# Kernel optimization log

Measured on AMD Instinct MI355X. Metric: run time of the kernel, lower is better.

Reference implementation:

```python
import jax, jax.numpy as jnp
import numpy as np

N = 32  # batch of graph samples; each has 5 frames x 4 nodes

def _conv(x, w, b):
    # x: [B,C,H,W], w: [O,I,3,3], stride 2, VALID
    y = jax.lax.conv_general_dilated(x, w, (2, 2), 'VALID',
                                     dimension_numbers=('NCHW', 'OIHW', 'NCHW'))
    return y + b[None, :, None, None]

def _pool(x):
    # MaxPool2d kernel 3 stride 3, VALID
    return jax.lax.reduce_window(x, -jnp.inf, jax.lax.max,
                                 (1, 1, 3, 3), (1, 1, 3, 3), 'VALID')

def _backbone(x, w1, b1, w2, b2, lw, lb):
    # x: [N*20, 3, 224, 224] -> [N,5,4,6]
    h = jax.nn.relu(_pool(_conv(x, w1, b1)))   # [N*20, 3, 37, 37]
    h = jax.nn.relu(_pool(_conv(h, w2, b2)))   # [N*20, 1, 6, 6]
    h = h.reshape(N, 5, 4, 36)
    return h @ lw + lb

def setup_inputs() -> dict:
    key = jax.random.key(0)
    ks = jax.random.split(key, 30)
    def rn(k, shape, s=0.05):
        return jax.random.normal(k, shape, dtype=jnp.float32) * s
    inp = {
        'nodes':  rn(ks[0], (N, 5, 4, 3, 224, 224), 1.0),
        'pos':    rn(ks[1], (N, 5, 4, 6), 1.0),
        'attmap': jax.random.uniform(ks[2], (N, 5, 4, 4), dtype=jnp.float32),
        'depths': rn(ks[3], (N, 5, 4, 3, 224, 224), 1.0),
        # RGB backbone params
        'c1w': rn(ks[4], (3, 3, 3, 3)),  'c1b': rn(ks[5], (3,)),
        'c2w': rn(ks[6], (1, 3, 3, 3)),  'c2b': rn(ks[7], (1,)),
        'lw':  rn(ks[8], (36, 6)),       'lb':  rn(ks[9], (6,)),
        # depth backbone params
        'dc1w': rn(ks[10], (3, 3, 3, 3)), 'dc1b': rn(ks[11], (3,)),
        'dc2w': rn(ks[12], (1, 3, 3, 3)), 'dc2b': rn(ks[13], (1,)),
        'dlw':  rn(ks[14], (36, 6)),      'dlb':  rn(ks[15], (6,)),
        # message-passing params
        'fmw': rn(ks[16], (6, 6)), 'fmb': rn(ks[17], (6,)),
        'lmw': rn(ks[18], (6, 6)), 'lmb': rn(ks[19], (6,)),
        # output MLP params
        'o1w': rn(ks[20], (360, 180)), 'o1b': rn(ks[21], (180,)),
        'o2w': rn(ks[22], (180, 60)),  'o2b': rn(ks[23], (60,)),
        'o3w': rn(ks[24], (60, 6)),    'o3b': rn(ks[25], (6,)),
    }
    return inp

def reference(nodes, pos, attmap, depths,
              c1w, c1b, c2w, c2b, lw, lb,
              dc1w, dc1b, dc2w, dc2b, dlw, dlb,
              fmw, fmb, lmw, lmb,
              o1w, o1b, o2w, o2b, o3w, o3b):
    nf = _backbone(nodes.reshape(N * 20, 3, 224, 224), c1w, c1b, c2w, c2b, lw, lb)    # [N,5,4,6]
    df = _backbone(depths.reshape(N * 20, 3, 224, 224), dc1w, dc1b, dc2w, dc2b, dlw, dlb)
    pm = pos @ fmw + fmb                                   # [N,5,4,6] per-frame messages
    msg = jnp.einsum('bfmn,bfmd->bfnd', attmap, pm)        # weighted sum over sender m
    prev = pos[:, :4] @ lmw + lmb                          # [N,4,4,6] contribution of frame f-1
    pos_up = msg.at[:, 1:].add(prev)                       # frame 0 has no temporal message
    feat = jnp.concatenate([nf, df, pos_up], axis=-1).reshape(N, 360)
    h = jax.nn.relu(feat @ o1w + o1b)
    h = jax.nn.relu(h @ o2w + o2b)
    return h @ o3w + o3b                                   # [N,6]
```

## Files before the change

### kernel.cpp

```cpp
#include <hip/hip_runtime.h>
#include <math.h>

#define NB 32
#define IMGS 640
#define HW 224
#define CHW (3*224*224)
#define P1 37
#define P1SQ (37*37)

__global__ __launch_bounds__(256) void stage1(
    const float* __restrict__ nodes, const float* __restrict__ depths,
    const float* __restrict__ c1w, const float* __restrict__ c1b,
    const float* __restrict__ dc1w, const float* __restrict__ dc1b,
    float* __restrict__ s1)
{
    const int bb = blockIdx.y;
    const int g = blockIdx.x * 256 + threadIdx.x;
    if (g >= IMGS * P1SQ) return;
    const int img = g / P1SQ;
    const int p   = g - img * P1SQ;
    const int ph  = p / P1;
    const int pw  = p - ph * P1;

    const float* __restrict__ x    = (bb ? depths : nodes) + (size_t)img * CHW;
    const float* __restrict__ w    = bb ? dc1w : c1w;
    const float* __restrict__ bias = bb ? dc1b : c1b;

    float acc[3][9];
    #pragma unroll
    for (int oc = 0; oc < 3; ++oc)
        #pragma unroll
        for (int q = 0; q < 9; ++q) acc[oc][q] = 0.f;

    const int row0 = 6 * ph;
    const int col0 = 6 * pw;

    #pragma unroll
    for (int i = 0; i < 3; ++i) {
        #pragma unroll
        for (int r = 0; r < 7; ++r) {
            const float2* rp = (const float2*)(x + (size_t)i*(HW*HW) + (size_t)(row0 + r)*HW + col0);
            const float2 v0 = rp[0], v1 = rp[1], v2 = rp[2], v3 = rp[3];
            const float row[8] = {v0.x, v0.y, v1.x, v1.y, v2.x, v2.y, v3.x, v3.y};
            #pragma unroll
            for (int dh = 0; dh < 3; ++dh) {
                const int kh = r - 2*dh;
                if (kh < 0 || kh > 2) continue;
                #pragma unroll
                for (int oc = 0; oc < 3; ++oc) {
                    #pragma unroll
                    for (int dw = 0; dw < 3; ++dw) {
                        #pragma unroll
                        for (int kw = 0; kw < 3; ++kw) {
                            acc[oc][dh*3+dw] += row[2*dw+kw] * w[((oc*3+i)*3+kh)*3+kw];
                        }
                    }
                }
            }
        }
    }

    #pragma unroll
    for (int oc = 0; oc < 3; ++oc) {
        float m = acc[oc][0];
        #pragma unroll
        for (int q = 1; q < 9; ++q) m = fmaxf(m, acc[oc][q]);
        m = fmaxf(m + bias[oc], 0.f);
        s1[(((size_t)bb*IMGS + img)*3 + oc)*P1SQ + p] = m;
    }
}

__global__ __launch_bounds__(128) void stage2(
    const float* __restrict__ s1,
    const float* __restrict__ c2w, const float* __restrict__ c2b,
    const float* __restrict__ dc2w, const float* __restrict__ dc2b,
    const float* __restrict__ lw, const float* __restrict__ lb,
    const float* __restrict__ dlw, const float* __restrict__ dlb,
    float* __restrict__ feats)
{
    const int bb  = blockIdx.x / IMGS;
    const int img = blockIdx.x - bb*IMGS;
    const float* __restrict__ w   = bb ? dc2w : c2w;
    const float* __restrict__ lwp = bb ? dlw : lw;
    const float* __restrict__ lbp = bb ? dlb : lb;
    const float b2 = (bb ? dc2b : c2b)[0];

    __shared__ float t1[3*P1SQ];
    __shared__ float v[36];

    const float* __restrict__ src = s1 + ((size_t)bb*IMGS + img)*3*P1SQ;
    for (int e = threadIdx.x; e < 3*P1SQ; e += 128) t1[e] = src[e];
    __syncthreads();

    const int t = threadIdx.x;
    if (t < 36) {
        const int py = t / 6, px = t - py*6;
        float m = -INFINITY;
        #pragma unroll
        for (int dh = 0; dh < 3; ++dh) {
            #pragma unroll
            for (int dw = 0; dw < 3; ++dw) {
                const int h = 3*py + dh, wv = 3*px + dw;
                float a = b2;
                #pragma unroll
                for (int i = 0; i < 3; ++i)
                    #pragma unroll
                    for (int kh = 0; kh < 3; ++kh)
                        #pragma unroll
                        for (int kw = 0; kw < 3; ++kw)
                            a += t1[i*P1SQ + (2*h+kh)*P1 + (2*wv+kw)] * w[(i*3+kh)*3+kw];
                m = fmaxf(m, a);
            }
        }
        v[t] = fmaxf(m, 0.f);
    }
    __syncthreads();
    if (t < 6) {
        float a = lbp[t];
        #pragma unroll
        for (int k = 0; k < 36; ++k) a += v[k] * lwp[k*6+t];
        feats[((size_t)bb*IMGS + img)*6 + t] = a;
    }
}

__global__ __launch_bounds__(192) void stage3(
    const float* __restrict__ pos, const float* __restrict__ att,
    const float* __restrict__ fmw, const float* __restrict__ fmb,
    const float* __restrict__ lmw, const float* __restrict__ lmb,
    const float* __restrict__ o1w, const float* __restrict__ o1b,
    const float* __restrict__ o2w, const float* __restrict__ o2b,
    const float* __restrict__ o3w, const float* __restrict__ o3b,
    const float* __restrict__ feats,
    float* __restrict__ out)
{
    const int n = blockIdx.x;
    const int t = threadIdx.x;
    __shared__ float feat[360];
    __shared__ float h1[180];
    __shared__ float h2[60];

    for (int u = t; u < 240; u += 192) {
        const int half = u / 120;
        const int idx  = u - half*120;
        const int fn   = idx / 6;
        const int j    = idx - fn*6;
        feat[fn*18 + half*6 + j] = feats[(size_t)half*(IMGS*6) + (n*20 + fn)*6 + j];
    }
    if (t < 120) {
        const int f    = t / 24;
        const int r    = t - f*24;
        const int node = r / 6;
        const int d    = r - node*6;
        float m = 0.f;
        #pragma unroll
        for (int mm = 0; mm < 4; ++mm) {
            float pmd = fmb[d];
            #pragma unroll
            for (int e = 0; e < 6; ++e)
                pmd += pos[(((size_t)n*5+f)*4+mm)*6+e] * fmw[e*6+d];
            m += att[(((size_t)n*5+f)*4+mm)*4+node] * pmd;
        }
        if (f >= 1) {
            float pv = lmb[d];
            #pragma unroll
            for (int e = 0; e < 6; ++e)
                pv += pos[(((size_t)n*5+(f-1))*4+node)*6+e] * lmw[e*6+d];
            m += pv;
        }
        feat[(f*4+node)*18 + 12 + d] = m;
    }
    __syncthreads();
    if (t < 180) {
        float a = o1b[t];
        for (int k = 0; k < 360; ++k) a += feat[k] * o1w[(size_t)k*180 + t];
        h1[t] = fmaxf(a, 0.f);
    }
    __syncthreads();
    if (t < 60) {
        float a = o2b[t];
        for (int k = 0; k < 180; ++k) a += h1[k] * o2w[k*60 + t];
        h2[t] = fmaxf(a, 0.f);
    }
    __syncthreads();
    if (t < 6) {
        float a = o3b[t];
        #pragma unroll
        for (int k = 0; k < 60; ++k) a += h2[k] * o3w[k*6 + t];
        out[n*6 + t] = a;
    }
}

extern "C" void kernel_launch(void* const* d_in, const int* in_sizes, int n_in,
                              void* d_out, int out_size, void* d_ws, size_t ws_size,
                              hipStream_t stream)
{
    const float* nodes  = (const float*)d_in[0];
    const float* pos    = (const float*)d_in[1];
    const float* att    = (const float*)d_in[2];
    const float* depths = (const float*)d_in[3];
    const float* c1w  = (const float*)d_in[4];
    const float* c1b  = (const float*)d_in[5];
    const float* c2w  = (const float*)d_in[6];
    const float* c2b  = (const float*)d_in[7];
    const float* lw   = (const float*)d_in[8];
    const float* lb   = (const float*)d_in[9];
    const float* dc1w = (const float*)d_in[10];
    const float* dc1b = (const float*)d_in[11];
    const float* dc2w = (const float*)d_in[12];
    const float* dc2b = (const float*)d_in[13];
    const float* dlw  = (const float*)d_in[14];
    const float* dlb  = (const float*)d_in[15];
    const float* fmw  = (const float*)d_in[16];
    const float* fmb  = (const float*)d_in[17];
    const float* lmw  = (const float*)d_in[18];
    const float* lmb  = (const float*)d_in[19];
    const float* o1w  = (const float*)d_in[20];
    const float* o1b  = (const float*)d_in[21];
    const float* o2w  = (const float*)d_in[22];
    const float* o2b  = (const float*)d_in[23];
    const float* o3w  = (const float*)d_in[24];
    const float* o3b  = (const float*)d_in[25];

    float* s1    = (float*)d_ws;
    float* feats = s1 + (size_t)2*IMGS*3*P1SQ;

    dim3 g1((IMGS*P1SQ + 255)/256, 2);
    stage1<<<g1, 256, 0, stream>>>(nodes, depths, c1w, c1b, dc1w, dc1b, s1);
    stage2<<<dim3(2*IMGS), 128, 0, stream>>>(s1, c2w, c2b, dc2w, dc2b,
                                             lw, lb, dlw, dlb, feats);
    stage3<<<dim3(NB), 192, 0, stream>>>(pos, att, fmw, fmb, lmw, lmb,
                                         o1w, o1b, o2w, o2b, o3w, o3b,
                                         feats, (float*)d_out);
}
```

Measured before the change: 794.8 us.

## Stage first conv through LDS strips with coalesced float4 loads

Restructures stage1 so each block handles one image strip of 12 output rows (plus one halo row) across all three channels. The strip is loaded into shared memory with coalesced float4 reads, and the conv weights and biases are staged in LDS too. Each thread then computes one output channel for one pooled pixel, replacing the old scheme where every thread fetched overlapping float2 rows from global memory and computed all three channels. The aim is to turn scattered global reads into bulk coalesced traffic. In exchange, blocks use about 35KB of LDS, which limits occupancy, some threads sit idle, strided LDS reads can hit bank conflicts, and the load and compute phases do not overlap.

```diff
diff --git a/kernel.cpp b/kernel.cpp
--- a/kernel.cpp
+++ b/kernel.cpp
@@ -7,6 +7,7 @@
 #define CHW (3*224*224)
 #define P1 37
 #define P1SQ (37*37)
+#define STRIPS 19
 
 __global__ __launch_bounds__(256) void stage1(
     const float* __restrict__ nodes, const float* __restrict__ depths,
@@ -14,59 +15,74 @@
     const float* __restrict__ dc1w, const float* __restrict__ dc1b,
     float* __restrict__ s1)
 {
-    const int bb = blockIdx.y;
-    const int g = blockIdx.x * 256 + threadIdx.x;
-    if (g >= IMGS * P1SQ) return;
-    const int img = g / P1SQ;
-    const int p   = g - img * P1SQ;
-    const int ph  = p / P1;
-    const int pw  = p - ph * P1;
+    const int img = blockIdx.x;
+    const int s   = blockIdx.y;
+    const int bb  = blockIdx.z;
+    const int t   = threadIdx.x;
 
     const float* __restrict__ x    = (bb ? depths : nodes) + (size_t)img * CHW;
     const float* __restrict__ w    = bb ? dc1w : c1w;
     const float* __restrict__ bias = bb ? dc1b : c1b;
 
-    float acc[3][9];
-    #pragma unroll
-    for (int oc = 0; oc < 3; ++oc)
-        #pragma unroll
-        for (int q = 0; q < 9; ++q) acc[oc][q] = 0.f;
-
-    const int row0 = 6 * ph;
-    const int col0 = 6 * pw;
-
-    #pragma unroll
-    for (int i = 0; i < 3; ++i) {
-        #pragma unroll
-        for (int r = 0; r < 7; ++r) {
-            const float2* rp = (const float2*)(x + (size_t)i*(HW*HW) + (size_t)(row0 + r)*HW + col0);
-            const float2 v0 = rp[0], v1 = rp[1], v2 = rp[2], v3 = rp[3];
-            const float row[8] = {v0.x, v0.y, v1.x, v1.y, v2.x, v2.y, v3.x, v3.y};
-            #pragma unroll
-            for (int dh = 0; dh < 3; ++dh) {
-                const int kh = r - 2*dh;
-                if (kh < 0 || kh > 2) continue;
+    __shared__ float tile[3*13*224];
+    __shared__ float wsm[81];
+    __shared__ float bsm[3];
+
+    if (t < 81) wsm[t] = w[t];
+    else if (t < 84) bsm[t-81] = bias[t-81];
+
+    const int r0 = 12 * s;
+    float4* lds4 = (float4*)tile;
+    const float4* g4 = (const float4*)x;
+    for (int f4 = t; f4 < 3*13*56; f4 += 256) {
+        const int ch = f4 / (13*56);
+        const int rr = (f4 / 56) % 13;
+        const int c4 = f4 - ch*(13*56) - rr*56;
+        const int row = r0 + rr;
+        if (row < HW)
+            lds4[f4] = g4[ch*(56*HW) + row*56 + c4];
+    }
+    __syncthreads();
+
+    const int nwork = (2*s + 1 < P1) ? 222 : 111;
+    if (t < nwork) {
+        const int sub = t / 111;
+        const int rem = t - sub*111;
+        const int oc  = rem / P1;
+        const int pw  = rem - oc*P1;
+        const int colb = 6*pw;
+        const int rb   = 6*sub;
+
+        float acc[9];
+        #pragma unroll
+        for (int q = 0; q < 9; ++q) acc[q] = 0.f;
+
+        #pragma unroll
+        for (int ch = 0; ch < 3; ++ch) {
+            #pragma unroll
+            for (int r = 0; r < 7; ++r) {
+                const float* rp = &tile[ch*(13*224) + (rb+r)*224 + colb];
+                float row[7];
                 #pragma unroll
-                for (int oc = 0; oc < 3; ++oc) {
+                for (int c = 0; c < 7; ++c) row[c] = rp[c];
+                #pragma unroll
+                for (int dh = 0; dh < 3; ++dh) {
+                    const int kh = r - 2*dh;
+                    if (kh < 0 || kh > 2) continue;
                     #pragma unroll
-                    for (int dw = 0; dw < 3; ++dw) {
+                    for (int dw = 0; dw < 3; ++dw)
                         #pragma unroll
-                        for (int kw = 0; kw < 3; ++kw) {
-                            acc[oc][dh*3+dw] += row[2*dw+kw] * w[((oc*3+i)*3+kh)*3+kw];
-                        }
-                    }
+                        for (int kw = 0; kw < 3; ++kw)
+                            acc[dh*3+dw] += row[2*dw+kw] * wsm[((oc*3+ch)*3+kh)*3+kw];
                 }
             }
         }
-    }
-
-    #pragma unroll
-    for (int oc = 0; oc < 3; ++oc) {
-        float m = acc[oc][0];
-        #pragma unroll
-        for (int q = 1; q < 9; ++q) m = fmaxf(m, acc[oc][q]);
-        m = fmaxf(m + bias[oc], 0.f);
-        s1[(((size_t)bb*IMGS + img)*3 + oc)*P1SQ + p] = m;
+        float m = acc[0];
+        #pragma unroll
+        for (int q = 1; q < 9; ++q) m = fmaxf(m, acc[q]);
+        m = fmaxf(m + bsm[oc], 0.f);
+        const int ph = 2*s + sub;
+        s1[(((size_t)bb*IMGS + img)*3 + oc)*P1SQ + ph*P1 + pw] = m;
     }
 }
 
@@ -224,8 +240,8 @@
     float* s1    = (float*)d_ws;
     float* feats = s1 + (size_t)2*IMGS*3*P1SQ;
 
-    dim3 g1((IMGS*P1SQ + 255)/256, 2);
-    stage1<<<g1, 256, 0, stream>>>(nodes, depths, c1w, c1b, dc1w, dc1b, s1);
+    stage1<<<dim3(IMGS, STRIPS, 2), 256, 0, stream>>>(nodes, depths,
+                                                      c1w, c1b, dc1w, dc1b, s1);
     stage2<<<dim3(2*IMGS), 128, 0, stream>>>(s1, c2w, c2b, dc2w, dc2b,
                                              lw, lb, dlw, dlb, feats);
     stage3<<<dim3(NB), 192, 0, stream>>>(pos, att, fmw, fmb, lmw, lmb,
```

After: 852.7 us. 1.07x slower.
